# Kernel tuning notes

Measured on AMD Instinct MI355X. Metric: run time of the kernel, lower is better.

## Reference

```python
import jax, jax.numpy as jnp
import numpy as np

N_NODES = 100000
N_EDGES = 600000
FEAT_DIM = 128


def setup_inputs() -> dict:
    key = jax.random.key(0)
    k_x, k_e, k_w1, k_b1, k_w2, k_b2 = jax.random.split(key, 6)
    x = jax.random.normal(k_x, (N_NODES, FEAT_DIM), dtype=jnp.float32)
    edge_index = jax.random.randint(k_e, (2, N_EDGES), 0, N_NODES, dtype=jnp.int64)
    # nn.Linear default init: U(-1/sqrt(fan_in), 1/sqrt(fan_in))
    lim1 = 1.0 / np.sqrt(2 * FEAT_DIM)
    lim2 = 1.0 / np.sqrt(FEAT_DIM)
    W1 = jax.random.uniform(k_w1, (2 * FEAT_DIM, FEAT_DIM), minval=-lim1, maxval=lim1, dtype=jnp.float32)
    b1 = jax.random.uniform(k_b1, (FEAT_DIM,), minval=-lim1, maxval=lim1, dtype=jnp.float32)
    W2 = jax.random.uniform(k_w2, (FEAT_DIM, 1), minval=-lim2, maxval=lim2, dtype=jnp.float32)
    b2 = jax.random.uniform(k_b2, (1,), minval=-lim2, maxval=lim2, dtype=jnp.float32)
    return {"x": x, "edge_index": edge_index, "W1": W1, "b1": b1, "W2": W2, "b2": b2}


def reference(x, edge_index, W1, b1, W2, b2):
    row, col = edge_index[0], edge_index[1]
    # gather endpoint features and concat -> [E, 2*feat_dim]
    edge_feat = jnp.concatenate([x[row], x[col]], axis=1)
    h = jax.nn.relu(edge_feat @ W1 + b1)  # [E, feat_dim]
    return jax.nn.sigmoid(h @ W2 + b2)    # [E, 1]
```

## Files before the change

kernel.cpp:

```cpp
#include <hip/hip_runtime.h>
#include <stdint.h>

#define N_NODES 100000
#define N_EDGES 600000
#define FEAT 128

typedef __attribute__((ext_vector_type(8))) short short8;
typedef __attribute__((ext_vector_type(4))) float floatx4;

__device__ __forceinline__ short f2bf(float f) {
    unsigned u = __builtin_bit_cast(unsigned, f);
    u = (u + 0x7FFFu + ((u >> 16) & 1u)) >> 16;
    return (short)u;
}
__device__ __forceinline__ float bf2f(short s) {
    unsigned u = ((unsigned)(unsigned short)s) << 16;
    return __builtin_bit_cast(float, u);
}

__global__ void cvt_w_kernel(const float* __restrict__ w1, short* __restrict__ wbt) {
    int i = blockIdx.x * 256 + threadIdx.x;
    int n = i >> 7, k = i & 127;
    float f = (n < FEAT) ? w1[k * FEAT + n] : w1[(FEAT + k) * FEAT + (n - FEAT)];
    wbt[i] = f2bf(f);
}

__global__ __launch_bounds__(256, 2) void node_gemm_kernel(
    const float* __restrict__ x, const short* __restrict__ wbt, short* __restrict__ y)
{
    __shared__ short lds_b[16 * 256 * 8];

    const int tid = threadIdx.x;
    for (int j = tid; j < 16 * 256; j += 256) {
        int n = j & 255, c = j >> 8;
        short8 v = *(const short8*)(wbt + n * 128 + c * 8);
        *(short8*)(lds_b + ((c << 8) + n) * 8) = v;
    }
    __syncthreads();

    const int lane = tid & 63;
    const int wave = tid >> 6;
    const int nl = lane & 15;
    const int q  = lane >> 4;
    const int m0 = blockIdx.x * 64 + wave * 16;

    const int node = m0 + nl;
    const int nsrc = (node < N_NODES) ? node : 0;
    short8 a[4];
#pragma unroll
    for (int s = 0; s < 4; ++s) {
        const float* p = x + (size_t)nsrc * FEAT + s * 32 + q * 8;
        short8 av;
#pragma unroll
        for (int j = 0; j < 8; ++j) av[j] = f2bf(p[j]);
        a[s] = av;
    }

    floatx4 acc[16];
#pragma unroll
    for (int nt = 0; nt < 16; ++nt) acc[nt] = (floatx4)(0.0f);

#pragma unroll
    for (int s = 0; s < 4; ++s) {
        const int crow = (s * 4 + q) << 8;
#pragma unroll
        for (int nt = 0; nt < 16; ++nt) {
            short8 bf = *(const short8*)(lds_b + ((crow + nt * 16 + nl) << 3));
            acc[nt] = __builtin_amdgcn_mfma_f32_16x16x32_bf16(a[s], bf, acc[nt], 0, 0, 0);
        }
    }

#pragma unroll
    for (int r = 0; r < 4; ++r) {
        int m = m0 + q * 4 + r;
        if (m >= N_NODES) continue;
        short* yr = y + (size_t)m * 256 + nl;
#pragma unroll
        for (int nt = 0; nt < 16; ++nt) yr[nt * 16] = f2bf(acc[nt][r]);
    }
}

__global__ __launch_bounds__(256) void edge_kernel(
    const short* __restrict__ y, const int* __restrict__ eidx,
    const float* __restrict__ b1, const float* __restrict__ w2,
    const float* __restrict__ b2, float* __restrict__ out)
{
    int t = blockIdx.x * 256 + threadIdx.x;
    int e = t >> 4;
    int l = t & 15;
    if (e >= N_EDGES) return;

    int r = eidx[e];
    int c = eidx[N_EDGES + e];

    short8 uu = *(const short8*)(y + (size_t)r * 256 + l * 8);
    short8 vv = *(const short8*)(y + (size_t)c * 256 + 128 + l * 8);

    const float* b1p = b1 + l * 8;
    const float* w2p = w2 + l * 8;

    float p = 0.0f;
#pragma unroll
    for (int j = 0; j < 8; ++j) {
        float h = bf2f(uu[j]) + bf2f(vv[j]) + b1p[j];
        p = fmaf(fmaxf(h, 0.0f), w2p[j], p);
    }
    p += __shfl_xor(p, 1);
    p += __shfl_xor(p, 2);
    p += __shfl_xor(p, 4);
    p += __shfl_xor(p, 8);

    if (l == 0) out[e] = 1.0f / (1.0f + __expf(-(p + b2[0])));
}

extern "C" void kernel_launch(void* const* d_in, const int* in_sizes, int n_in,
                              void* d_out, int out_size, void* d_ws, size_t ws_size,
                              hipStream_t stream) {
    const float* x  = (const float*)d_in[0];
    const int*   ei = (const int*)d_in[1];
    const float* W1 = (const float*)d_in[2];
    const float* b1 = (const float*)d_in[3];
    const float* W2 = (const float*)d_in[4];
    const float* b2 = (const float*)d_in[5];
    float* out = (float*)d_out;

    short* ybf = (short*)d_ws;
    short* wbt = ybf + (size_t)N_NODES * 256;

    cvt_w_kernel<<<32768 / 256, 256, 0, stream>>>(W1, wbt);

    int mblocks = (N_NODES + 63) / 64;
    node_gemm_kernel<<<mblocks, 256, 0, stream>>>(x, wbt, ybf);

    int eblocks = (N_EDGES * 16) / 256;
    edge_kernel<<<eblocks, 256, 0, stream>>>(ybf, ei, b1, W2, b2, out);
}
```

Before: 168.0 us.

## Fuse weight conversion into persistent GEMM, permute output layout, vectorize edge kernel

```diff
diff --git a/kernel.cpp b/kernel.cpp
--- a/kernel.cpp
+++ b/kernel.cpp
@@ -4,37 +4,44 @@
 #define N_NODES 100000
 #define N_EDGES 600000
 #define FEAT 128
+#define NTILES ((N_NODES + 63) / 64)
+#define GEMM_BLOCKS 512
+#define EDGE_BLOCKS 2048
 
 typedef __attribute__((ext_vector_type(8))) short short8;
 typedef __attribute__((ext_vector_type(4))) float floatx4;
 
-__device__ __forceinline__ short f2bf(float f) {
+__device__ __forceinline__ unsigned f2bf_u(float f) {
     unsigned u = __builtin_bit_cast(unsigned, f);
-    u = (u + 0x7FFFu + ((u >> 16) & 1u)) >> 16;
-    return (short)u;
-}
-__device__ __forceinline__ float bf2f(short s) {
-    unsigned u = ((unsigned)(unsigned short)s) << 16;
-    return __builtin_bit_cast(float, u);
-}
-
-__global__ void cvt_w_kernel(const float* __restrict__ w1, short* __restrict__ wbt) {
-    int i = blockIdx.x * 256 + threadIdx.x;
-    int n = i >> 7, k = i & 127;
-    float f = (n < FEAT) ? w1[k * FEAT + n] : w1[(FEAT + k) * FEAT + (n - FEAT)];
-    wbt[i] = f2bf(f);
-}
+    return (u + 0x7FFFu + ((u >> 16) & 1u)) >> 16;
+}
+__device__ __forceinline__ short f2bf(float f) { return (short)f2bf_u(f); }
+__device__ __forceinline__ float bflo(int w) {
+    return __builtin_bit_cast(float, (unsigned)w << 16);
+}
+__device__ __forceinline__ float bfhi(int w) {
+    return __builtin_bit_cast(float, (unsigned)w & 0xFFFF0000u);
+}
+
 
 __global__ __launch_bounds__(256, 2) void node_gemm_kernel(
-    const float* __restrict__ x, const short* __restrict__ wbt, short* __restrict__ y)
+    const float* __restrict__ x, const float* __restrict__ w1,
+    const float* __restrict__ b1, const float* __restrict__ w2,
+    short* __restrict__ y, float2* __restrict__ pw)
 {
     __shared__ short lds_b[16 * 256 * 8];
 
     const int tid = threadIdx.x;
-    for (int j = tid; j < 16 * 256; j += 256) {
-        int n = j & 255, c = j >> 8;
-        short8 v = *(const short8*)(wbt + n * 128 + c * 8);
-        *(short8*)(lds_b + ((c << 8) + n) * 8) = v;
+
+    if (blockIdx.x == 0 && tid < 128) {
+        int j = (tid & 7) * 16 + (tid >> 3);
+        pw[tid] = make_float2(b1[j], w2[j]);
+    }
+
+    for (int i = tid; i < 32768; i += 256) {
+        int k = i >> 8, n = i & 255;
+        float f = (n < FEAT) ? w1[k * FEAT + n] : w1[(FEAT + k) * FEAT + (n - FEAT)];
+        lds_b[(((k >> 3) << 8) + n) * 8 + (k & 7)] = f2bf(f);
     }
     __syncthreads();
 
@@ -42,75 +49,142 @@
     const int wave = tid >> 6;
     const int nl = lane & 15;
     const int q  = lane >> 4;
-    const int m0 = blockIdx.x * 64 + wave * 16;
-
-    const int node = m0 + nl;
-    const int nsrc = (node < N_NODES) ? node : 0;
-    short8 a[4];
-#pragma unroll
-    for (int s = 0; s < 4; ++s) {
-        const float* p = x + (size_t)nsrc * FEAT + s * 32 + q * 8;
-        short8 av;
-#pragma unroll
-        for (int j = 0; j < 8; ++j) av[j] = f2bf(p[j]);
-        a[s] = av;
-    }
-
-    floatx4 acc[16];
-#pragma unroll
-    for (int nt = 0; nt < 16; ++nt) acc[nt] = (floatx4)(0.0f);
-
-#pragma unroll
-    for (int s = 0; s < 4; ++s) {
-        const int crow = (s * 4 + q) << 8;
-#pragma unroll
-        for (int nt = 0; nt < 16; ++nt) {
-            short8 bf = *(const short8*)(lds_b + ((crow + nt * 16 + nl) << 3));
-            acc[nt] = __builtin_amdgcn_mfma_f32_16x16x32_bf16(a[s], bf, acc[nt], 0, 0, 0);
-        }
-    }
-
-#pragma unroll
-    for (int r = 0; r < 4; ++r) {
-        int m = m0 + q * 4 + r;
-        if (m >= N_NODES) continue;
-        short* yr = y + (size_t)m * 256 + nl;
-#pragma unroll
-        for (int nt = 0; nt < 16; ++nt) yr[nt * 16] = f2bf(acc[nt][r]);
-    }
+
+    int t = blockIdx.x;
+    float4 cur[8];
+    if (t < NTILES) {
+        int node = t * 64 + wave * 16 + nl;
+        int nsrc = node < N_NODES ? node : N_NODES - 1;
+        const float* bp = x + (size_t)nsrc * FEAT + q * 8;
+#pragma unroll
+        for (int s = 0; s < 4; ++s) {
+            cur[2 * s]     = *(const float4*)(bp + s * 32);
+            cur[2 * s + 1] = *(const float4*)(bp + s * 32 + 4);
+        }
+    }
+
+    for (; t < NTILES; ) {
+        int tn = t + GEMM_BLOCKS;
+        float4 nxt[8];
+        if (tn < NTILES) {
+            int node = tn * 64 + wave * 16 + nl;
+            int nsrc = node < N_NODES ? node : N_NODES - 1;
+            const float* bp = x + (size_t)nsrc * FEAT + q * 8;
+#pragma unroll
+            for (int s = 0; s < 4; ++s) {
+                nxt[2 * s]     = *(const float4*)(bp + s * 32);
+                nxt[2 * s + 1] = *(const float4*)(bp + s * 32 + 4);
+            }
+        }
+
+        short8 a[4];
+#pragma unroll
+        for (int s = 0; s < 4; ++s) {
+            const float* f0 = (const float*)&cur[2 * s];
+            const float* f1 = (const float*)&cur[2 * s + 1];
+            short8 av;
+            av[0] = f2bf(f0[0]); av[1] = f2bf(f0[1]); av[2] = f2bf(f0[2]); av[3] = f2bf(f0[3]);
+            av[4] = f2bf(f1[0]); av[5] = f2bf(f1[1]); av[6] = f2bf(f1[2]); av[7] = f2bf(f1[3]);
+            a[s] = av;
+        }
+
+        floatx4 acc[16];
+#pragma unroll
+        for (int nt = 0; nt < 16; ++nt) acc[nt] = (floatx4)(0.0f);
+
+#pragma unroll
+        for (int s = 0; s < 4; ++s) {
+            const int crow = (s * 4 + q) << 8;
+#pragma unroll
+            for (int nt = 0; nt < 16; ++nt) {
+                short8 bf = *(const short8*)(lds_b + ((crow + nt * 16 + nl) << 3));
+                acc[nt] = __builtin_amdgcn_mfma_f32_16x16x32_bf16(a[s], bf, acc[nt], 0, 0, 0);
+            }
+        }
+
+        const int m0 = t * 64 + wave * 16;
+#pragma unroll
+        for (int r = 0; r < 4; ++r) {
+            int m = m0 + q * 4 + r;
+            if (m < N_NODES) {
+                int up[4], vp[4];
+#pragma unroll
+                for (int d = 0; d < 4; ++d) {
+                    up[d] = (int)(f2bf_u(acc[2 * d][r])     | (f2bf_u(acc[2 * d + 1][r]) << 16));
+                    vp[d] = (int)(f2bf_u(acc[8 + 2 * d][r]) | (f2bf_u(acc[9 + 2 * d][r]) << 16));
+                }
+                short* yr = y + (size_t)m * 256 + nl * 8;
+                *(int4*)yr         = make_int4(up[0], up[1], up[2], up[3]);
+                *(int4*)(yr + 128) = make_int4(vp[0], vp[1], vp[2], vp[3]);
+            }
+        }
+
+#pragma unroll
+        for (int s = 0; s < 8; ++s) cur[s] = nxt[s];
+        t = tn;
+    }
+}
+
+__device__ __forceinline__ float dotacc(int4 u, int4 v, const float2* pwr, int base, float p) {
+    int uu[4] = {u.x, u.y, u.z, u.w};
+    int vv[4] = {v.x, v.y, v.z, v.w};
+#pragma unroll
+    for (int d = 0; d < 4; ++d) {
+        float h0 = bflo(uu[d]) + bflo(vv[d]) + pwr[base + 2 * d].x;
+        float h1 = bfhi(uu[d]) + bfhi(vv[d]) + pwr[base + 2 * d + 1].x;
+        p = fmaf(fmaxf(h0, 0.0f), pwr[base + 2 * d].y, p);
+        p = fmaf(fmaxf(h1, 0.0f), pwr[base + 2 * d + 1].y, p);
+    }
+    return p;
 }
 
 __global__ __launch_bounds__(256) void edge_kernel(
     const short* __restrict__ y, const int* __restrict__ eidx,
-    const float* __restrict__ b1, const float* __restrict__ w2,
-    const float* __restrict__ b2, float* __restrict__ out)
+    const float2* __restrict__ pw, const float* __restrict__ b2,
+    float* __restrict__ out)
 {
-    int t = blockIdx.x * 256 + threadIdx.x;
-    int e = t >> 4;
-    int l = t & 15;
-    if (e >= N_EDGES) return;
-
-    int r = eidx[e];
-    int c = eidx[N_EDGES + e];
-
-    short8 uu = *(const short8*)(y + (size_t)r * 256 + l * 8);
-    short8 vv = *(const short8*)(y + (size_t)c * 256 + 128 + l * 8);
-
-    const float* b1p = b1 + l * 8;
-    const float* w2p = w2 + l * 8;
-
-    float p = 0.0f;
-#pragma unroll
-    for (int j = 0; j < 8; ++j) {
-        float h = bf2f(uu[j]) + bf2f(vv[j]) + b1p[j];
-        p = fmaf(fmaxf(h, 0.0f), w2p[j], p);
-    }
-    p += __shfl_xor(p, 1);
-    p += __shfl_xor(p, 2);
-    p += __shfl_xor(p, 4);
-    p += __shfl_xor(p, 8);
-
-    if (l == 0) out[e] = 1.0f / (1.0f + __expf(-(p + b2[0])));
+    const int gt = blockIdx.x * 256 + threadIdx.x;
+    const int l = gt & 7;
+    const int g = gt >> 3;
+    const int G = (EDGE_BLOCKS * 256) / 8;
+
+    float2 pwr[16];
+#pragma unroll
+    for (int i = 0; i < 16; ++i) pwr[i] = pw[l * 16 + i];
+    const float bias2 = b2[0];
+
+    for (int e = g; e < N_EDGES; e += 2 * G) {
+        int e2 = e + G;
+        bool h2 = e2 < N_EDGES;
+        int r1 = eidx[e];
+        int c1 = eidx[N_EDGES + e];
+        int r2 = h2 ? eidx[e2] : 0;
+        int c2 = h2 ? eidx[N_EDGES + e2] : 0;
+
+        const short* u1p = y + (size_t)r1 * 256 + l * 16;
+        const short* v1p = y + (size_t)c1 * 256 + 128 + l * 16;
+        const short* u2p = y + (size_t)r2 * 256 + l * 16;
+        const short* v2p = y + (size_t)c2 * 256 + 128 + l * 16;
+        int4 ua1 = *(const int4*)u1p, ub1 = *(const int4*)(u1p + 8);
+        int4 va1 = *(const int4*)v1p, vb1 = *(const int4*)(v1p + 8);
+        int4 ua2 = *(const int4*)u2p, ub2 = *(const int4*)(u2p + 8);
+        int4 va2 = *(const int4*)v2p, vb2 = *(const int4*)(v2p + 8);
+
+        float p1 = 0.0f, p2 = 0.0f;
+        p1 = dotacc(ua1, va1, pwr, 0, p1);
+        p1 = dotacc(ub1, vb1, pwr, 8, p1);
+        p2 = dotacc(ua2, va2, pwr, 0, p2);
+        p2 = dotacc(ub2, vb2, pwr, 8, p2);
+
+        p1 += __shfl_xor(p1, 1);  p2 += __shfl_xor(p2, 1);
+        p1 += __shfl_xor(p1, 2);  p2 += __shfl_xor(p2, 2);
+        p1 += __shfl_xor(p1, 4);  p2 += __shfl_xor(p2, 4);
+
+        if (l == 0) {
+            out[e] = 1.0f / (1.0f + __expf(-(p1 + bias2)));
+            if (h2) out[e2] = 1.0f / (1.0f + __expf(-(p2 + bias2)));
+        }
+    }
 }
 
 extern "C" void kernel_launch(void* const* d_in, const int* in_sizes, int n_in,
@@ -124,14 +198,9 @@
     const float* b2 = (const float*)d_in[5];
     float* out = (float*)d_out;
 
-    short* ybf = (short*)d_ws;
-    short* wbt = ybf + (size_t)N_NODES * 256;
-
-    cvt_w_kernel<<<32768 / 256, 256, 0, stream>>>(W1, wbt);
-
-    int mblocks = (N_NODES + 63) / 64;
-    node_gemm_kernel<<<mblocks, 256, 0, stream>>>(x, wbt, ybf);
-
-    int eblocks = (N_EDGES * 16) / 256;
-    edge_kernel<<<eblocks, 256, 0, stream>>>(ybf, ei, b1, W2, b2, out);
-}
+    short*  ybf = (short*)d_ws;
+    float2* pw  = (float2*)(ybf + (size_t)N_NODES * 256);
+
+    node_gemm_kernel<<<GEMM_BLOCKS, 256, 0, stream>>>(x, W1, b1, W2, ybf, pw);
+    edge_kernel<<<EDGE_BLOCKS, 256, 0, stream>>>(ybf, ei, pw, b2, out);
+}
```

Measured after the change: 213.9 us. 27.3% more time.
